# Performance work log

Measured on AMD Instinct MI355X. Metric: run time of the kernel, lower is better.

The kernel has to match this reference:

```python
import jax, jax.numpy as jnp
import numpy as np

N = 50000
E = 800000
NEG_SLOPE = 0.2


def setup_inputs() -> dict:
    key = jax.random.key(0)
    ks = jax.random.split(key, 12)
    feat = jax.random.normal(ks[0], (N, 256), dtype=jnp.float32)
    src = jax.random.randint(ks[1], (E,), 0, N, dtype=jnp.int32)
    dst = jax.random.randint(ks[2], (E,), 0, N, dtype=jnp.int32)
    # layer 1: in=256 -> H=4, D=64 (concat 256)
    W1 = jax.random.normal(ks[3], (256, 256), dtype=jnp.float32) * (1.0 / np.sqrt(256))
    attn_l1 = jax.random.normal(ks[4], (4, 64), dtype=jnp.float32) * 0.1
    attn_r1 = jax.random.normal(ks[5], (4, 64), dtype=jnp.float32) * 0.1
    bias1 = jnp.zeros((256,), dtype=jnp.float32)
    # layer 2: in=256 -> H=1, D=128
    W2 = jax.random.normal(ks[6], (256, 128), dtype=jnp.float32) * (1.0 / np.sqrt(256))
    attn_l2 = jax.random.normal(ks[7], (1, 128), dtype=jnp.float32) * 0.1
    attn_r2 = jax.random.normal(ks[8], (1, 128), dtype=jnp.float32) * 0.1
    bias2 = jnp.zeros((128,), dtype=jnp.float32)
    return {"feat": feat, "src": src, "dst": dst,
            "W1": W1, "attn_l1": attn_l1, "attn_r1": attn_r1, "bias1": bias1,
            "W2": W2, "attn_l2": attn_l2, "attn_r2": attn_r2, "bias2": bias2}


def gat_conv(feat, src, dst, W, attn_l, attn_r, bias, apply_relu):
    H, D = attn_l.shape
    n = feat.shape[0]
    ft = (feat @ W).reshape(n, H, D)                      # [N,H,D]
    el = jnp.einsum('nhd,hd->nh', ft, attn_l)             # [N,H]
    er = jnp.einsum('nhd,hd->nh', ft, attn_r)             # [N,H]
    e = el[src] + er[dst]                                 # [E,H]  u_add_v
    e = jnp.where(e > 0, e, NEG_SLOPE * e)                # leaky_relu
    # edge softmax grouped by dst
    m = jax.ops.segment_max(e, dst, num_segments=n)       # [N,H]
    ex = jnp.exp(e - m[dst])
    denom = jax.ops.segment_sum(ex, dst, num_segments=n)  # [N,H]
    a = ex / denom[dst]                                   # [E,H]
    msg = ft[src] * a[:, :, None]                         # [E,H,D]
    out = jax.ops.segment_sum(msg, dst, num_segments=n)   # [N,H,D]
    out = out + bias.reshape(1, H, D)
    out = out.reshape(n, H * D)                           # concat_out
    if apply_relu:
        out = jax.nn.relu(out)
    return out


def reference(feat, src, dst, W1, attn_l1, attn_r1, bias1, W2, attn_l2, attn_r2, bias2):
    h = gat_conv(feat, src, dst, W1, attn_l1, attn_r1, bias1, apply_relu=True)
    h = gat_conv(h, src, dst, W2, attn_l2, attn_r2, bias2, apply_relu=False)
    return h
```

## Files before the change

kernel.cpp:

```cpp
#include <hip/hip_runtime.h>

#define NEG_SLOPE 0.2f
#define BIN_CAP 8192

typedef short s16x8 __attribute__((ext_vector_type(8)));
typedef float f32x4 __attribute__((ext_vector_type(4)));
typedef float f32x2 __attribute__((ext_vector_type(2)));

typedef __attribute__((address_space(3))) unsigned int lds_u32;
typedef __attribute__((address_space(1))) const unsigned int glb_u32;

__device__ __forceinline__ unsigned short f2bf(float f) {
    unsigned int u = __float_as_uint(f);
    unsigned int r = (u + 0x7fffu + ((u >> 16) & 1u)) >> 16;
    return (unsigned short)r;
}
__device__ __forceinline__ float bf2f(unsigned int us) {
    return __uint_as_float(us << 16);
}


__global__ __launch_bounds__(256) void binpart_k(
        const int* __restrict__ src, const int* __restrict__ dst, int E,
        int* __restrict__ bin_cur, int* __restrict__ ovf_n,
        int2* __restrict__ pairs,
        int* __restrict__ ovf_dst, int* __restrict__ ovf_src,
        const float* __restrict__ W1, const float* __restrict__ al1,
        const float* __restrict__ ar1,
        const float* __restrict__ W2, const float* __restrict__ al2,
        const float* __restrict__ ar2,
        float* __restrict__ wl1, float* __restrict__ wl2,
        unsigned short* __restrict__ Bt1h, unsigned short* __restrict__ Bt1l,
        unsigned short* __restrict__ Bt2h, unsigned short* __restrict__ Bt2l) {
    const int b = blockIdx.x;
    if (b == 0) {
        int k = threadIdx.x;
        #pragma unroll
        for (int h = 0; h < 4; h++) {
            float sl = 0.f, sr = 0.f;
            #pragma unroll 8
            for (int d = 0; d < 64; d++) {
                float wv = W1[k * 256 + h * 64 + d];
                sl = fmaf(wv, al1[h * 64 + d], sl);
                sr = fmaf(wv, ar1[h * 64 + d], sr);
            }
            wl1[k * 8 + h] = sl;
            wl1[k * 8 + 4 + h] = sr;
        }
        float sl = 0.f, sr = 0.f;
        #pragma unroll 8
        for (int d = 0; d < 128; d++) {
            float wv = W2[k * 128 + d];
            sl = fmaf(wv, al2[d], sl);
            sr = fmaf(wv, ar2[d], sr);
        }
        wl2[k * 2 + 0] = sl;
        wl2[k * 2 + 1] = sr;
        return;
    }
    if (b <= 4) {
        int c = (b - 1) * 64 + (threadIdx.x >> 2);
        int kq = threadIdx.x & 3;
        #pragma unroll 8
        for (int kk = 0; kk < 64; kk++) {
            int k = kq + kk * 4;
            float w = W1[k * 256 + c];
            unsigned short h = f2bf(w);
            unsigned short l = f2bf(w - bf2f(h));
            Bt1h[c * 256 + k] = h;
            Bt1l[c * 256 + k] = l;
        }
        return;
    }
    if (b <= 6) {
        int c = (b - 5) * 64 + (threadIdx.x >> 2);
        int kq = threadIdx.x & 3;
        #pragma unroll 8
        for (int kk = 0; kk < 64; kk++) {
            int k = kq + kk * 4;
            float w = W2[k * 128 + c];
            unsigned short h = f2bf(w);
            unsigned short l = f2bf(w - bf2f(h));
            Bt2h[c * 256 + k] = h;
            Bt2l[c * 256 + k] = l;
        }
        return;
    }
    __shared__ int l_cnt[256];
    __shared__ int l_base[256];
    const int tid = threadIdx.x;
    const int base_e = (b - 7) * 2048 + tid * 8;
    int s[8], d[8], bn[8], rk[8];
    bool v[8];
    if (base_e + 7 < E) {
        int4 a0 = *(const int4*)(src + base_e);
        int4 a1 = *(const int4*)(src + base_e + 4);
        int4 c0 = *(const int4*)(dst + base_e);
        int4 c1 = *(const int4*)(dst + base_e + 4);
        s[0]=a0.x; s[1]=a0.y; s[2]=a0.z; s[3]=a0.w;
        s[4]=a1.x; s[5]=a1.y; s[6]=a1.z; s[7]=a1.w;
        d[0]=c0.x; d[1]=c0.y; d[2]=c0.z; d[3]=c0.w;
        d[4]=c1.x; d[5]=c1.y; d[6]=c1.z; d[7]=c1.w;
        #pragma unroll
        for (int i = 0; i < 8; i++) v[i] = true;
    } else {
        #pragma unroll
        for (int i = 0; i < 8; i++) {
            int e = base_e + i;
            v[i] = e < E;
            s[i] = v[i] ? src[e] : 0;
            d[i] = v[i] ? dst[e] : 0;
        }
    }
    l_cnt[tid] = 0;
    __syncthreads();
    #pragma unroll
    for (int i = 0; i < 8; i++) {
        bn[i] = d[i] >> 8;
        if (v[i]) rk[i] = atomicAdd(&l_cnt[bn[i]], 1);
    }
    __syncthreads();
    {
        int c = l_cnt[tid];
        if (c > 0) l_base[tid] = atomicAdd(&bin_cur[tid * 16], c);
    }
    __syncthreads();
    #pragma unroll
    for (int i = 0; i < 8; i++) {
        if (v[i]) {
            int pos = l_base[bn[i]] + rk[i];
            if (pos < BIN_CAP) {
                int2 p; p.x = s[i]; p.y = d[i];
                pairs[(size_t)bn[i] * BIN_CAP + pos] = p;
            } else {
                int j = atomicAdd(ovf_n, 1);
                ovf_dst[j] = d[i]; ovf_src[j] = s[i];
            }
        }
    }
}


__global__ __launch_bounds__(256) void prepfill_k(
        const int* __restrict__ bin_cur, const int2* __restrict__ pairs,
        int* __restrict__ cnt, int* __restrict__ bucket,
        int* __restrict__ ovf_n, int* __restrict__ ovf_dst, int* __restrict__ ovf_src,
        const float* __restrict__ feat, const float* __restrict__ wl1,
        unsigned short* __restrict__ Ah, unsigned short* __restrict__ Al,
        float* __restrict__ el1, float* __restrict__ er1, int Nn, int nbin) {
    if ((int)blockIdx.x < nbin) {
        __shared__ int l_cnt[256];
        const int b = blockIdx.x;
        const int tid = threadIdx.x;
        l_cnt[tid] = 0;
        __syncthreads();
        const int ec = min(bin_cur[b * 16], BIN_CAP);
        const int2* pp = pairs + (size_t)b * BIN_CAP;
        for (int i = tid; i < ec; i += 256) {
            int2 p = pp[i];
            int pos = atomicAdd(&l_cnt[p.y & 255], 1);
            if (pos < 64) bucket[((size_t)p.y << 6) + pos] = p.x;
            else {
                int j = atomicAdd(ovf_n, 1);
                ovf_dst[j] = p.y; ovf_src[j] = p.x;
            }
        }
        __syncthreads();
        int node = b * 256 + tid;
        if (node < Nn) cnt[node] = l_cnt[tid];
        return;
    }
    const int lane = threadIdx.x & 63, wid = threadIdx.x >> 6;
    const int n = ((int)blockIdx.x - nbin) * 4 + wid;
    if (n >= Nn) return;
    float4 f = ((const float4*)(feat + (size_t)n * 256))[lane];
    unsigned short h0 = f2bf(f.x), h1 = f2bf(f.y), h2 = f2bf(f.z), h3 = f2bf(f.w);
    unsigned short l0 = f2bf(f.x - bf2f(h0)), l1 = f2bf(f.y - bf2f(h1));
    unsigned short l2 = f2bf(f.z - bf2f(h2)), l3 = f2bf(f.w - bf2f(h3));
    uint2 hv, lv;
    hv.x = (unsigned)h0 | ((unsigned)h1 << 16);
    hv.y = (unsigned)h2 | ((unsigned)h3 << 16);
    lv.x = (unsigned)l0 | ((unsigned)l1 << 16);
    lv.y = (unsigned)l2 | ((unsigned)l3 << 16);
    ((uint2*)(Ah + (size_t)n * 256))[lane] = hv;
    ((uint2*)(Al + (size_t)n * 256))[lane] = lv;

    float ff[4] = {f.x, f.y, f.z, f.w};
    float pa[4] = {0.f, 0.f, 0.f, 0.f}, pb[4] = {0.f, 0.f, 0.f, 0.f};
    const float* wp = wl1 + lane * 32;
    #pragma unroll
    for (int j = 0; j < 4; j++) {
        float4 wa = *(const float4*)(wp + j * 8);
        float4 wb = *(const float4*)(wp + j * 8 + 4);
        pa[0] = fmaf(ff[j], wa.x, pa[0]); pa[1] = fmaf(ff[j], wa.y, pa[1]);
        pa[2] = fmaf(ff[j], wa.z, pa[2]); pa[3] = fmaf(ff[j], wa.w, pa[3]);
        pb[0] = fmaf(ff[j], wb.x, pb[0]); pb[1] = fmaf(ff[j], wb.y, pb[1]);
        pb[2] = fmaf(ff[j], wb.z, pb[2]); pb[3] = fmaf(ff[j], wb.w, pb[3]);
    }
    #pragma unroll
    for (int h = 0; h < 4; h++) {
        #pragma unroll
        for (int o = 32; o > 0; o >>= 1) {
            pa[h] += __shfl_xor(pa[h], o);
            pb[h] += __shfl_xor(pb[h], o);
        }
    }
    if (lane == 0) {
        ((float4*)el1)[n] = float4{pa[0], pa[1], pa[2], pa[3]};
        ((float4*)er1)[n] = float4{pb[0], pb[1], pb[2], pb[3]};
    }
}


__global__ __launch_bounds__(256) void gemm_k(const unsigned short* __restrict__ Ah,
                                              const unsigned short* __restrict__ Al,
                                              const unsigned short* __restrict__ Bh,
                                              const unsigned short* __restrict__ Bl,
                                              unsigned short* __restrict__ Cb,
                                              int M, int Nc) {
    __shared__ __align__(16) unsigned short SB[12288];

    const int tid = threadIdx.x;
    const int lane = tid & 63, wid = tid >> 6;
    const int row0 = blockIdx.y * 128;
    const int col0 = blockIdx.x * 64;
    const int wm = (wid & 1) * 64;
    const int wn = (wid >> 1) * 32;
    const int quad = lane >> 4, mrow = lane & 15;

    const unsigned short* gb[6];
    unsigned ldsoff[6];
    {
        const int lr = lane >> 2;
        const int kc = (lane & 3) * 8;
        #pragma unroll
        for (int j = 0; j < 6; j++) {
            int c = wid * 6 + j;
            const unsigned short* base;
            int row;
            if (c < 8)       { base = Ah; row = min(row0 + c * 16 + lr, M - 1); }
            else if (c < 16) { base = Al; row = min(row0 + (c - 8) * 16 + lr, M - 1); }
            else if (c < 20) { base = Bh; row = col0 + (c - 16) * 16 + lr; }
            else             { base = Bl; row = col0 + (c - 20) * 16 + lr; }
            gb[j] = base + (size_t)row * 256 + kc;
            ldsoff[j] = (unsigned)c * 512;
        }
    }

    f32x4 acc[4][2];
    #pragma unroll
    for (int i = 0; i < 4; i++)
        #pragma unroll
        for (int j = 0; j < 2; j++) acc[i][j] = f32x4{0.f, 0.f, 0.f, 0.f};

    for (int kt = 0; kt < 8; kt++) {
        __syncthreads();
        #pragma unroll
        for (int j = 0; j < 6; j++) {
            __builtin_amdgcn_global_load_lds((glb_u32*)(gb[j] + kt * 32),
                                             (lds_u32*)&SB[ldsoff[j]], 16, 0, 0);
        }
        __syncthreads();

        s16x8 ah[4], al4[4], bh[2], bl[2];
        #pragma unroll
        for (int i = 0; i < 4; i++) {
            int r = wm + 16 * i + mrow;
            ah[i]  = *(const s16x8*)&SB[r * 32 + quad * 8];
            al4[i] = *(const s16x8*)&SB[4096 + r * 32 + quad * 8];
        }
        #pragma unroll
        for (int j = 0; j < 2; j++) {
            int r = wn + 16 * j + mrow;
            bh[j] = *(const s16x8*)&SB[8192 + r * 32 + quad * 8];
            bl[j] = *(const s16x8*)&SB[10240 + r * 32 + quad * 8];
        }
        #pragma unroll
        for (int i = 0; i < 4; i++)
            #pragma unroll
            for (int j = 0; j < 2; j++) {
                acc[i][j] = __builtin_amdgcn_mfma_f32_16x16x32_bf16(ah[i],  bh[j], acc[i][j], 0, 0, 0);
                acc[i][j] = __builtin_amdgcn_mfma_f32_16x16x32_bf16(ah[i],  bl[j], acc[i][j], 0, 0, 0);
                acc[i][j] = __builtin_amdgcn_mfma_f32_16x16x32_bf16(al4[i], bh[j], acc[i][j], 0, 0, 0);
            }
    }

    #pragma unroll
    for (int i = 0; i < 4; i++) {
        #pragma unroll
        for (int j = 0; j < 2; j++) {
            int col = col0 + wn + 16 * j + mrow;
            int rbase = row0 + wm + 16 * i + quad * 4;
            #pragma unroll
            for (int r = 0; r < 4; r++) {
                int row = rbase + r;
                if (row < M) Cb[(size_t)row * Nc + col] = f2bf(acc[i][j][r]);
            }
        }
    }
}


__device__ __forceinline__ void fma8(f32x2* acc, float wgt, uint4 u) {
    f32x2 w2; w2.x = wgt; w2.y = wgt;
    f32x2 p;
    p.x = __uint_as_float(u.x << 16); p.y = __uint_as_float(u.x & 0xffff0000u);
    acc[0] = p * w2 + acc[0];
    p.x = __uint_as_float(u.y << 16); p.y = __uint_as_float(u.y & 0xffff0000u);
    acc[1] = p * w2 + acc[1];
    p.x = __uint_as_float(u.z << 16); p.y = __uint_as_float(u.z & 0xffff0000u);
    acc[2] = p * w2 + acc[2];
    p.x = __uint_as_float(u.w << 16); p.y = __uint_as_float(u.w & 0xffff0000u);
    acc[3] = p * w2 + acc[3];
}

template <int H, int D, bool RELU, bool FUSE2>
__global__ __launch_bounds__(256) void fagg_k(const unsigned short* __restrict__ ft,
                                              const float* __restrict__ el,
                                              const float* __restrict__ er,
                                              const int* __restrict__ cnt,
                                              const int* __restrict__ bucket,
                                              const int* __restrict__ ovf_n,
                                              const int* __restrict__ ovf_dst,
                                              const int* __restrict__ ovf_src,
                                              const float* __restrict__ bias,
                                              float* __restrict__ out, int n_nodes,
                                              unsigned short* __restrict__ oh,
                                              unsigned short* __restrict__ ol,
                                              const float* __restrict__ wl2,
                                              float* __restrict__ el2,
                                              float* __restrict__ er2) {
    constexpr int HD = H * D;
    constexpr int LPE = HD / 8;
    constexpr int EPI = 64 / LPE;
    constexpr int SH = (HD == 256) ? 9 : 8;
    const int lane = threadIdx.x & 63;
    const int w = threadIdx.x >> 6;
    const int n = blockIdx.x * 4 + w;
    __shared__ int   s_src[4][64];
    __shared__ float s_a[4][64 * H];
    if (n >= n_nodes) return;
    const int deg = cnt[n];
    const int novf = *ovf_n;
    const int lane_sub = lane & (LPE - 1);
    const int q = lane / LPE;
    const int c0 = lane_sub * 8;
    const int h_of = c0 / D;
    const unsigned lsub16 = (unsigned)(lane_sub * 16);
    const char* fb = (const char*)ft;
    const char* eb = (const char*)el;

    float ern[H];
    #pragma unroll
    for (int h = 0; h < H; h++) ern[h] = er[n * H + h];

    f32x2 acc[4];
    #pragma unroll
    for (int t = 0; t < 4; t++) acc[t] = f32x2{0.f, 0.f};

    const int* s_src_w = s_src[w];
    const float* s_a_w = s_a[w];

    if (deg <= 64 && novf == 0) {
        const bool act = lane < deg;
        int sv = act ? bucket[(n << 6) + lane] : 0;
        s_src[w][lane] = sv;
        float evr[H];
        if constexpr (H == 4) {
            float4 e4 = *(const float4*)(eb + ((unsigned)sv << 4));
            evr[0] = e4.x; evr[1] = e4.y; evr[2] = e4.z; evr[3] = e4.w;
        } else {
            evr[0] = *(const float*)(eb + ((unsigned)sv << 2));
        }
        const int rc = (deg + EPI - 1) & ~(EPI - 1);
        const int nl = rc / EPI;
        const int nl0 = nl < 16 ? nl : 16;
        uint4 vv[8];
        #pragma unroll
        for (int i = 0; i < 8; i++) {
            if (i < nl0) {
                unsigned bo = ((unsigned)s_src_w[i * EPI + q] << SH) + lsub16;
                vv[i] = *(const uint4*)(fb + bo);
            }
        }
        float ex[H], sm[H];
        #pragma unroll
        for (int h = 0; h < H; h++) {
            float t = evr[h] + ern[h];
            t = t > 0.f ? t : NEG_SLOPE * t;
            ex[h] = act ? __expf(t) : 0.f;
            sm[h] = ex[h];
        }
        #pragma unroll
        for (int h = 0; h < H; h++)
            for (int o = 32; o > 0; o >>= 1) sm[h] += __shfl_xor(sm[h], o);
        #pragma unroll
        for (int h = 0; h < H; h++)
            s_a[w][lane * H + h] = ex[h] * (sm[h] > 0.f ? 1.f / sm[h] : 0.f);
        #pragma unroll
        for (int i = 0; i < 16; i++) {
            if (i < nl0) {
                float wt = s_a_w[(i * EPI + q) * H + h_of];
                fma8(acc, wt, vv[i & 7]);
                if (i + 8 < nl0) {
                    unsigned bo = ((unsigned)s_src_w[(i + 8) * EPI + q] << SH) + lsub16;
                    vv[i & 7] = *(const uint4*)(fb + bo);
                }
            }
        }
        for (int e = 16 * EPI + q; e < rc; e += EPI) {
            unsigned bo = ((unsigned)s_src_w[e] << SH) + lsub16;
            uint4 v = *(const uint4*)(fb + bo);
            fma8(acc, s_a_w[e * H + h_of], v);
        }
    } else {
        const int bval = deg < 64 ? deg : 64;
        const bool act = lane < bval;
        int sv0 = act ? bucket[(n << 6) + lane] : 0;
        s_src[w][lane] = sv0;
        float sm[H];
        #pragma unroll
        for (int h = 0; h < H; h++) sm[h] = 0.f;
        {
            float evr[H];
            if constexpr (H == 4) {
                float4 e4 = ((const float4*)el)[sv0];
                evr[0] = e4.x; evr[1] = e4.y; evr[2] = e4.z; evr[3] = e4.w;
            } else evr[0] = el[sv0];
            #pragma unroll
            for (int h = 0; h < H; h++) {
                float t = evr[h] + ern[h];
                t = t > 0.f ? t : NEG_SLOPE * t;
                if (act) sm[h] += __expf(t);
            }
        }
        for (int i = lane; i < novf; i += 64) {
            if (ovf_dst[i] == n) {
                int sv = ovf_src[i];
                float evr[H];
                if constexpr (H == 4) {
                    float4 e4 = ((const float4*)el)[sv];
                    evr[0] = e4.x; evr[1] = e4.y; evr[2] = e4.z; evr[3] = e4.w;
                } else evr[0] = el[sv];
                #pragma unroll
                for (int h = 0; h < H; h++) {
                    float t = evr[h] + ern[h];
                    t = t > 0.f ? t : NEG_SLOPE * t;
                    sm[h] += __expf(t);
                }
            }
        }
        #pragma unroll
        for (int h = 0; h < H; h++)
            for (int o = 32; o > 0; o >>= 1) sm[h] += __shfl_xor(sm[h], o);
        float inv[H];
        #pragma unroll
        for (int h = 0; h < H; h++) inv[h] = (sm[h] > 0.f) ? (1.f / sm[h]) : 0.f;
        {
            float evr[H];
            if constexpr (H == 4) {
                float4 e4 = ((const float4*)el)[sv0];
                evr[0] = e4.x; evr[1] = e4.y; evr[2] = e4.z; evr[3] = e4.w;
            } else evr[0] = el[sv0];
            #pragma unroll
            for (int h = 0; h < H; h++) {
                float t = evr[h] + ern[h];
                t = t > 0.f ? t : NEG_SLOPE * t;
                s_a[w][lane * H + h] = act ? __expf(t) * inv[h] : 0.f;
            }
        }
        for (int e = q; e < 64; e += EPI) {
            unsigned bo = ((unsigned)s_src_w[e] << SH) + lsub16;
            uint4 v = *(const uint4*)(fb + bo);
            fma8(acc, s_a_w[e * H + h_of], v);
        }
        for (int i = 0; i < novf; i++) {
            if (ovf_dst[i] != n) continue;
            int sv = ovf_src[i];
            float elh, ernh, invh;
            if constexpr (H == 4) {
                float4 e4 = ((const float4*)el)[sv];
                elh  = (h_of & 2) ? ((h_of & 1) ? e4.w : e4.z)
                                  : ((h_of & 1) ? e4.y : e4.x);
                ernh = (h_of & 2) ? ((h_of & 1) ? ern[3] : ern[2])
                                  : ((h_of & 1) ? ern[1] : ern[0]);
                invh = (h_of & 2) ? ((h_of & 1) ? inv[3] : inv[2])
                                  : ((h_of & 1) ? inv[1] : inv[0]);
            } else {
                elh = el[sv]; ernh = ern[0]; invh = inv[0];
            }
            float t = elh + ernh;
            t = t > 0.f ? t : NEG_SLOPE * t;
            float wt = __expf(t) * invh;
            uint4 v = *(const uint4*)(fb + (((unsigned)sv << SH) + lsub16));
            if (q == 0) fma8(acc, wt, v);
        }
    }

    float accs[8];
    #pragma unroll
    for (int t = 0; t < 8; t++) accs[t] = acc[t >> 1][t & 1];

    #pragma unroll
    for (int t = 0; t < 8; t++) {
        #pragma unroll
        for (int s = LPE; s < 64; s <<= 1) accs[t] += __shfl_xor(accs[t], s);
    }
    if (lane < LPE) {
        float4 b0 = ((const float4*)bias)[lane * 2];
        float4 b1 = ((const float4*)bias)[lane * 2 + 1];
        float v[8] = {accs[0] + b0.x, accs[1] + b0.y, accs[2] + b0.z, accs[3] + b0.w,
                      accs[4] + b1.x, accs[5] + b1.y, accs[6] + b1.z, accs[7] + b1.w};
        if (RELU) {
            #pragma unroll
            for (int t = 0; t < 8; t++) v[t] = fmaxf(v[t], 0.f);
        }
        if constexpr (FUSE2) {
            unsigned short hh[8], ll[8];
            #pragma unroll
            for (int t = 0; t < 8; t++) {
                hh[t] = f2bf(v[t]);
                ll[t] = f2bf(v[t] - bf2f(hh[t]));
            }
            uint4 hv, lv;
            hv.x = (unsigned)hh[0] | ((unsigned)hh[1] << 16);
            hv.y = (unsigned)hh[2] | ((unsigned)hh[3] << 16);
            hv.z = (unsigned)hh[4] | ((unsigned)hh[5] << 16);
            hv.w = (unsigned)hh[6] | ((unsigned)hh[7] << 16);
            lv.x = (unsigned)ll[0] | ((unsigned)ll[1] << 16);
            lv.y = (unsigned)ll[2] | ((unsigned)ll[3] << 16);
            lv.z = (unsigned)ll[4] | ((unsigned)ll[5] << 16);
            lv.w = (unsigned)ll[6] | ((unsigned)ll[7] << 16);
            ((uint4*)(oh + (size_t)n * HD))[lane] = hv;
            ((uint4*)(ol + (size_t)n * HD))[lane] = lv;
            float pa = 0.f, pb = 0.f;
            #pragma unroll
            for (int t = 0; t < 8; t++) {
                float2 wv = ((const float2*)wl2)[lane * 8 + t];
                pa = fmaf(v[t], wv.x, pa);
                pb = fmaf(v[t], wv.y, pb);
            }
            #pragma unroll
            for (int o = 16; o > 0; o >>= 1) {
                pa += __shfl_xor(pa, o);
                pb += __shfl_xor(pb, o);
            }
            if (lane == 0) { el2[n] = pa; er2[n] = pb; }
        } else {
            float4 o0{v[0], v[1], v[2], v[3]};
            float4 o1{v[4], v[5], v[6], v[7]};
            float4* op = (float4*)out + (size_t)n * (HD / 4) + lane * 2;
            op[0] = o0;
            op[1] = o1;
        }
    }
}


extern "C" void kernel_launch(void* const* d_in, const int* in_sizes, int n_in,
                              void* d_out, int out_size, void* d_ws, size_t ws_size,
                              hipStream_t stream) {
    const float* feat    = (const float*)d_in[0];
    const int*   src     = (const int*)d_in[1];
    const int*   dst     = (const int*)d_in[2];
    const float* W1      = (const float*)d_in[3];
    const float* attn_l1 = (const float*)d_in[4];
    const float* attn_r1 = (const float*)d_in[5];
    const float* bias1   = (const float*)d_in[6];
    const float* W2      = (const float*)d_in[7];
    const float* attn_l2 = (const float*)d_in[8];
    const float* attn_r2 = (const float*)d_in[9];
    const float* bias2   = (const float*)d_in[10];
    float* out = (float*)d_out;

    const int N = in_sizes[0] / 256;
    const int E = in_sizes[1];
    const int nbin = (N + 255) >> 8;
    const int nbP = (E + 2047) / 2048;

    char* ws = (char*)d_ws;
    size_t o = 0;
    auto alloc = [&](size_t bytes) -> void* {
        void* p = ws + o;
        o = (o + bytes + 255) & ~(size_t)255;
        return p;
    };
    int* bin_cur = (int*)alloc(((size_t)nbin * 16 + 64) * 4);
    int* ovf_n   = bin_cur + (size_t)nbin * 16;
    int* cnt     = (int*)alloc((size_t)N * 4);
    int* bucket  = (int*)alloc((size_t)N * 64 * 4);
    int* ovf_dst = (int*)alloc((size_t)E * 4);
    int* ovf_src = (int*)alloc((size_t)E * 4);
    float* wl1 = (float*)alloc(256 * 8 * 4);
    float* wl2 = (float*)alloc(256 * 2 * 4);
    float* el1 = (float*)alloc((size_t)N * 4 * 4);
    float* er1 = (float*)alloc((size_t)N * 4 * 4);
    float* el2 = (float*)alloc((size_t)N * 4);
    float* er2 = (float*)alloc((size_t)N * 4);
    unsigned short* ft1b = (unsigned short*)alloc((size_t)N * 256 * 2);
    unsigned short* Ah   = (unsigned short*)alloc((size_t)N * 256 * 2);
    unsigned short* Al   = (unsigned short*)alloc((size_t)N * 256 * 2);
    unsigned short* Bt1h = (unsigned short*)alloc((size_t)256 * 256 * 2);
    unsigned short* Bt1l = (unsigned short*)alloc((size_t)256 * 256 * 2);
    unsigned short* Bt2h = (unsigned short*)alloc((size_t)128 * 256 * 2);
    unsigned short* Bt2l = (unsigned short*)alloc((size_t)128 * 256 * 2);
    unsigned short* ft2b = ft1b;
    unsigned short* h1h  = Ah;
    unsigned short* h1l  = Al;
    int2* pairs = (int2*)ft1b;

    hipMemsetAsync(bin_cur, 0, ((size_t)nbin * 16 + 64) * 4, stream);
    binpart_k<<<7 + nbP, 256, 0, stream>>>(src, dst, E, bin_cur, ovf_n, pairs,
                                           ovf_dst, ovf_src,
                                           W1, attn_l1, attn_r1, W2, attn_l2, attn_r2,
                                           wl1, wl2, Bt1h, Bt1l, Bt2h, Bt2l);
    prepfill_k<<<nbin + (N + 3) / 4, 256, 0, stream>>>(bin_cur, pairs, cnt, bucket,
                                                       ovf_n, ovf_dst, ovf_src,
                                                       feat, wl1, Ah, Al, el1, er1, N, nbin);

    gemm_k<<<dim3(4, (N + 127) / 128), 256, 0, stream>>>(Ah, Al, Bt1h, Bt1l, ft1b, N, 256);
    fagg_k<4, 64, true, true><<<(N + 3) / 4, 256, 0, stream>>>(ft1b, el1, er1, cnt, bucket,
                                                               ovf_n, ovf_dst, ovf_src,
                                                               bias1, nullptr, N,
                                                               h1h, h1l, wl2, el2, er2);

    gemm_k<<<dim3(2, (N + 127) / 128), 256, 0, stream>>>(h1h, h1l, Bt2h, Bt2l, ft2b, N, 128);
    fagg_k<1, 128, false, false><<<(N + 3) / 4, 256, 0, stream>>>(ft2b, el2, er2, cnt, bucket,
                                                                  ovf_n, ovf_dst, ovf_src,
                                                                  bias2, out, N,
                                                                  nullptr, nullptr, nullptr,
                                                                  nullptr, nullptr);
}
```

Measured before the change: 349.5 us.

## Shard edge-partition bin counters and unroll fixed gather loads in aggregation

```diff
diff --git a/kernel.cpp b/kernel.cpp
--- a/kernel.cpp
+++ b/kernel.cpp
@@ -1,7 +1,7 @@
 #include <hip/hip_runtime.h>
 
 #define NEG_SLOPE 0.2f
-#define BIN_CAP 8192
+#define SHARD_CAP 1024
 
 typedef short s16x8 __attribute__((ext_vector_type(8)));
 typedef float f32x4 __attribute__((ext_vector_type(4)));
@@ -89,7 +89,9 @@
     __shared__ int l_cnt[256];
     __shared__ int l_base[256];
     const int tid = threadIdx.x;
-    const int base_e = (b - 7) * 2048 + tid * 8;
+    const int pb = b - 7;
+    const int shard = pb & 7;
+    const int base_e = pb * 2048 + tid * 8;
     int s[8], d[8], bn[8], rk[8];
     bool v[8];
     if (base_e + 7 < E) {
@@ -122,16 +124,16 @@
     __syncthreads();
     {
         int c = l_cnt[tid];
-        if (c > 0) l_base[tid] = atomicAdd(&bin_cur[tid * 16], c);
+        if (c > 0) l_base[tid] = atomicAdd(&bin_cur[(tid * 8 + shard) * 16], c);
     }
     __syncthreads();
     #pragma unroll
     for (int i = 0; i < 8; i++) {
         if (v[i]) {
             int pos = l_base[bn[i]] + rk[i];
-            if (pos < BIN_CAP) {
+            if (pos < SHARD_CAP) {
                 int2 p; p.x = s[i]; p.y = d[i];
-                pairs[(size_t)bn[i] * BIN_CAP + pos] = p;
+                pairs[(((size_t)bn[i] * 8 + shard) << 10) + pos] = p;
             } else {
                 int j = atomicAdd(ovf_n, 1);
                 ovf_dst[j] = d[i]; ovf_src[j] = s[i];
@@ -154,15 +156,18 @@
         const int tid = threadIdx.x;
         l_cnt[tid] = 0;
         __syncthreads();
-        const int ec = min(bin_cur[b * 16], BIN_CAP);
-        const int2* pp = pairs + (size_t)b * BIN_CAP;
-        for (int i = tid; i < ec; i += 256) {
-            int2 p = pp[i];
-            int pos = atomicAdd(&l_cnt[p.y & 255], 1);
-            if (pos < 64) bucket[((size_t)p.y << 6) + pos] = p.x;
-            else {
-                int j = atomicAdd(ovf_n, 1);
-                ovf_dst[j] = p.y; ovf_src[j] = p.x;
+        #pragma unroll
+        for (int sh = 0; sh < 8; sh++) {
+            const int ec = min(bin_cur[(b * 8 + sh) * 16], SHARD_CAP);
+            const int2* pp = pairs + (((size_t)b * 8 + sh) << 10);
+            for (int i = tid; i < ec; i += 256) {
+                int2 p = pp[i];
+                int pos = atomicAdd(&l_cnt[p.y & 255], 1);
+                if (pos < 64) bucket[((size_t)p.y << 6) + pos] = p.x;
+                else {
+                    int j = atomicAdd(ovf_n, 1);
+                    ovf_dst[j] = p.y; ovf_src[j] = p.x;
+                }
             }
         }
         __syncthreads();
@@ -361,6 +366,9 @@
     const int* s_src_w = s_src[w];
     const float* s_a_w = s_a[w];
 
+#define GLD(i) (*(const uint4*)(fb + (((unsigned)s_src_w[(i) * EPI + q] << SH) + lsub16)))
+#define WT(i)  (s_a_w[((i) * EPI + q) * H + h_of])
+
     if (deg <= 64 && novf == 0) {
         const bool act = lane < deg;
         int sv = act ? bucket[(n << 6) + lane] : 0;
@@ -372,17 +380,9 @@
         } else {
             evr[0] = *(const float*)(eb + ((unsigned)sv << 2));
         }
-        const int rc = (deg + EPI - 1) & ~(EPI - 1);
-        const int nl = rc / EPI;
-        const int nl0 = nl < 16 ? nl : 16;
-        uint4 vv[8];
-        #pragma unroll
-        for (int i = 0; i < 8; i++) {
-            if (i < nl0) {
-                unsigned bo = ((unsigned)s_src_w[i * EPI + q] << SH) + lsub16;
-                vv[i] = *(const uint4*)(fb + bo);
-            }
-        }
+        const int nl = (deg + EPI - 1) / EPI;
+        uint4 v0 = GLD(0), v1 = GLD(1), v2 = GLD(2), v3 = GLD(3);
+        uint4 v4 = GLD(4), v5 = GLD(5), v6 = GLD(6), v7 = GLD(7);
         float ex[H], sm[H];
         #pragma unroll
         for (int h = 0; h < H; h++) {
@@ -397,21 +397,17 @@
         #pragma unroll
         for (int h = 0; h < H; h++)
             s_a[w][lane * H + h] = ex[h] * (sm[h] > 0.f ? 1.f / sm[h] : 0.f);
-        #pragma unroll
-        for (int i = 0; i < 16; i++) {
-            if (i < nl0) {
-                float wt = s_a_w[(i * EPI + q) * H + h_of];
-                fma8(acc, wt, vv[i & 7]);
-                if (i + 8 < nl0) {
-                    unsigned bo = ((unsigned)s_src_w[(i + 8) * EPI + q] << SH) + lsub16;
-                    vv[i & 7] = *(const uint4*)(fb + bo);
-                }
-            }
-        }
-        for (int e = 16 * EPI + q; e < rc; e += EPI) {
-            unsigned bo = ((unsigned)s_src_w[e] << SH) + lsub16;
-            uint4 v = *(const uint4*)(fb + bo);
-            fma8(acc, s_a_w[e * H + h_of], v);
+        fma8(acc, WT(0), v0); fma8(acc, WT(1), v1);
+        fma8(acc, WT(2), v2); fma8(acc, WT(3), v3);
+        fma8(acc, WT(4), v4); fma8(acc, WT(5), v5);
+        fma8(acc, WT(6), v6); fma8(acc, WT(7), v7);
+        constexpr int MAXNL = 64 / EPI;
+        #pragma unroll
+        for (int i0 = 8; i0 < MAXNL; i0 += 4) {
+            if (i0 >= nl) break;
+            uint4 a = GLD(i0), b2 = GLD(i0 + 1), c2 = GLD(i0 + 2), d2 = GLD(i0 + 3);
+            fma8(acc, WT(i0), a);     fma8(acc, WT(i0 + 1), b2);
+            fma8(acc, WT(i0 + 2), c2); fma8(acc, WT(i0 + 3), d2);
         }
     } else {
         const int bval = deg < 64 ? deg : 64;
@@ -496,6 +492,8 @@
             if (q == 0) fma8(acc, wt, v);
         }
     }
+#undef GLD
+#undef WT
 
     float accs[8];
     #pragma unroll
@@ -585,8 +583,8 @@
         o = (o + bytes + 255) & ~(size_t)255;
         return p;
     };
-    int* bin_cur = (int*)alloc(((size_t)nbin * 16 + 64) * 4);
-    int* ovf_n   = bin_cur + (size_t)nbin * 16;
+    int* bin_cur = (int*)alloc(((size_t)nbin * 8 * 16 + 64) * 4);
+    int* ovf_n   = bin_cur + (size_t)nbin * 8 * 16;
     int* cnt     = (int*)alloc((size_t)N * 4);
     int* bucket  = (int*)alloc((size_t)N * 64 * 4);
     int* ovf_dst = (int*)alloc((size_t)E * 4);
@@ -609,7 +607,7 @@
     unsigned short* h1l  = Al;
     int2* pairs = (int2*)ft1b;
 
-    hipMemsetAsync(bin_cur, 0, ((size_t)nbin * 16 + 64) * 4, stream);
+    hipMemsetAsync(bin_cur, 0, ((size_t)nbin * 8 * 16 + 64) * 4, stream);
     binpart_k<<<7 + nbP, 256, 0, stream>>>(src, dst, E, bin_cur, ovf_n, pairs,
                                            ovf_dst, ovf_src,
                                            W1, attn_l1, attn_r1, W2, attn_l2, attn_r2,
```

After: 341.4 us. 1.02x faster.
